# Optimization experiments

Measured on AMD Instinct MI355X. Metric: run time of the kernel, lower is better.

Reference implementation:

```python
import jax, jax.numpy as jnp
import numpy as np

N = 10000      # nodes
E = 160000     # edges (avg degree 16)
H = 128        # hidden_size
L = 3          # n_layers
NRBF = 20
RADIUS = 5.0
EPS = 1e-8
MAXZ = 100


def _xav(k, shape):
    fan_in = shape[-2]
    return jax.random.normal(k, shape, jnp.float32) / jnp.sqrt(jnp.float32(fan_in))


def setup_inputs() -> dict:
    key = jax.random.key(0)
    ks = jax.random.split(key, 12)
    return {
        "z": jax.random.randint(ks[0], (N,), 0, MAXZ, dtype=jnp.int32),
        "edge_vec": jax.random.normal(ks[1], (E, 3), jnp.float32),
        "senders": jax.random.randint(ks[2], (E,), 0, N, dtype=jnp.int32),
        "receivers": jax.random.randint(ks[3], (E,), 0, N, dtype=jnp.int32),
        "emb": jax.random.uniform(ks[4], (MAXZ, H), jnp.float32, -0.1, 0.1),
        "filt_W": _xav(ks[5], (NRBF, L * 3 * H)),
        "filt_b": jnp.zeros((L * 3 * H,), jnp.float32),
        "iW1": _xav(ks[6], (L, H, H)),
        "ib1": jnp.zeros((L, H), jnp.float32),
        "iW2": _xav(ks[7], (L, H, 3 * H)),
        "ib2": jnp.zeros((L, 3 * H), jnp.float32),
        "mW1": _xav(ks[8], (L, 2 * H, H)),
        "mb1": jnp.zeros((L, H), jnp.float32),
        "mW2": _xav(ks[9], (L, H, 3 * H)),
        "mb2": jnp.zeros((L, 3 * H), jnp.float32),
        "vW": _xav(ks[10], (L, H, 2 * H)),
    }


def _painn(z, edge_vec, senders, receivers, emb, filt_W, filt_b,
           iW1, ib1, iW2, ib2, mW1, mb1, mW2, mb2, vW):
    n = z.shape[0]
    clip = lambda x: jnp.clip(x, -1e4, 1e4)

    # edge geometry: norm + direction
    d = jnp.sqrt(jnp.sum(edge_vec ** 2, axis=-1, keepdims=True) + EPS)  # [E,1]
    dir_ij = edge_vec / d                                               # [E,3]

    # gaussian radial basis + cosine cutoff
    mu = jnp.linspace(0.0, RADIUS, NRBF)
    gamma = 0.5 / (RADIUS / NRBF) ** 2
    phi = jnp.exp(-gamma * (d - mu) ** 2)                               # [E,NRBF]
    cut = 0.5 * (jnp.cos(jnp.pi * d / RADIUS) + 1.0) * (d < RADIUS)     # [E,1]

    filters = (phi @ filt_W + filt_b) * cut                             # [E, L*3H]
    filt = jnp.split(filters, L, axis=-1)

    # embed
    s = emb[z]                                                          # [N,H]
    v = jnp.zeros((n, 3, H), dtype=s.dtype)                             # [N,3,H]

    for l in range(L):
        # ---- message ----
        x = jax.nn.silu(s @ iW1[l] + ib1[l]) @ iW2[l] + ib2[l]          # [N,3H]
        m = filt[l] * x[receivers]                                      # [E,3H]
        ds, dv1, dv2 = jnp.split(m, 3, axis=-1)
        dv = dv1[:, None, :] * dir_ij[:, :, None] + dv2[:, None, :] * v[receivers]  # [E,3,H]
        ds = jax.ops.segment_sum(ds, senders, num_segments=n)
        dv = jax.ops.segment_sum(dv, senders, num_segments=n)
        s = s + clip(ds)
        v = v + clip(dv)
        # ---- update / mixing ----
        v_l, v_r = jnp.split(v @ vW[l], 2, axis=-1)                     # [N,3,H] each
        v_norm = jnp.sqrt(jnp.sum(v_l ** 2, axis=-2) + EPS)             # [N,H]
        ts = jnp.concatenate([s, v_norm], axis=-1)                      # [N,2H]
        mm = jax.nn.silu(ts @ mW1[l] + mb1[l]) @ mW2[l] + mb2[l]        # [N,3H]
        ds2, dvu, dsv = jnp.split(mm, 3, axis=-1)
        s = s + clip(ds2 + dsv * jnp.sum(v_l * v_r, axis=1))
        v = v + clip(dvu[:, None, :] * v_r)
    return s, v


def reference(z, edge_vec, senders, receivers, emb, filt_W, filt_b,
              iW1, ib1, iW2, ib2, mW1, mb1, mW2, mb2, vW):
    return _painn(z, edge_vec, senders, receivers, emb, filt_W, filt_b,
                  iW1, ib1, iW2, ib2, mW1, mb1, mW2, mb2, vW)
```

## Files before the change

kernel.cpp:

```cpp
#include <hip/hip_runtime.h>
#include <math.h>

#define NN 10000
#define EE 160000
#define H 128
#define LAYERS 3
#define NRBF 20
#define RADIUS 5.0f
#define PI_F 3.14159265358979323846f

using f16    = _Float16;
using h2     = __attribute__((ext_vector_type(2)))  _Float16;
using half8  = __attribute__((ext_vector_type(8)))  _Float16;
using f32x16 = __attribute__((ext_vector_type(16))) float;
using u32x4  = __attribute__((ext_vector_type(4)))  unsigned int;

__device__ __forceinline__ float clipf(float x){ return fminf(fmaxf(x, -1e4f), 1e4f); }
__device__ __forceinline__ float siluf(float x){ return x / (1.0f + __expf(-x)); }

__global__ __launch_bounds__(256) void hist_kernel(const int* __restrict__ send, int* __restrict__ cnt){
    int e = blockIdx.x * 256 + threadIdx.x;
    if (e < EE) atomicAdd(&cnt[send[e]], 1);
}

__global__ __launch_bounds__(1024) void scan_kernel(const int* __restrict__ cnt,
                                                    int* __restrict__ row_ptr,
                                                    int* __restrict__ cursor){
    __shared__ int part[1024];
    int t = threadIdx.x;
    int base = t * 10;
    int local[10];
    int sum = 0;
    #pragma unroll
    for (int i = 0; i < 10; i++){
        int idx = base + i;
        local[i] = (idx < NN) ? cnt[idx] : 0;
        sum += local[i];
    }
    part[t] = sum;
    __syncthreads();
    for (int off = 1; off < 1024; off <<= 1){
        int val = (t >= off) ? part[t - off] : 0;
        __syncthreads();
        part[t] += val;
        __syncthreads();
    }
    int run = (t > 0) ? part[t-1] : 0;
    #pragma unroll
    for (int i = 0; i < 10; i++){
        int idx = base + i;
        if (idx < NN){ row_ptr[idx] = run; cursor[idx] = run; run += local[i]; }
    }
    if (t == 1023) row_ptr[NN] = part[1023];
}

__global__ __launch_bounds__(256) void build_kernel(const float* __restrict__ ev,
                                                    const int* __restrict__ send,
                                                    const int* __restrict__ recv,
                                                    int* __restrict__ cursor,
                                                    int* __restrict__ recv_s,
                                                    f16* __restrict__ Ps){
    int e = blockIdx.x * 256 + threadIdx.x;
    if (e >= EE) return;
    int p = atomicAdd(&cursor[send[e]], 1);
    recv_s[p] = recv[e];
    float x = ev[e*3+0], y = ev[e*3+1], z = ev[e*3+2];
    float d = sqrtf(x*x + y*y + z*z + 1e-8f);
    float inv = 1.0f / d;
    float cut = (d < RADIUS) ? 0.5f * (__cosf(PI_F * d / RADIUS) + 1.0f) : 0.0f;
    union { u32x4 q[3]; f16 h[24]; } o;
    #pragma unroll
    for (int k = 0; k < NRBF; k++){
        float mu = RADIUS * (float)k / (float)(NRBF - 1);
        float t = d - mu;
        o.h[k] = (f16)(__expf(-8.0f * t * t) * cut);
    }
    o.h[20] = (f16)cut;
    o.h[21] = (f16)(x*inv); o.h[22] = (f16)(y*inv); o.h[23] = (f16)(z*inv);
    u32x4* dst = (u32x4*)(Ps + (size_t)p*24);
    dst[0] = o.q[0]; dst[1] = o.q[1]; dst[2] = o.q[2];
}

__global__ __launch_bounds__(256) void wconv_kernel(const float* __restrict__ iW1, const float* __restrict__ iW2,
                                                    const float* __restrict__ vW,  const float* __restrict__ mW1,
                                                    const float* __restrict__ mW2,
                                                    f16* __restrict__ iW1T, f16* __restrict__ iW2T,
                                                    f16* __restrict__ vWT,  f16* __restrict__ mW1T,
                                                    f16* __restrict__ mW2T){
    int idx = blockIdx.x*256 + threadIdx.x;
    if (idx >= 3*180224) return;
    int l = idx / 180224;
    int r = idx % 180224;
    float val; f16* dst;
    if (r < 16384){
        int n = r >> 7, k = r & 127;
        val = iW1[l*16384 + k*128 + n]; dst = iW1T + l*16384 + r;
    } else if (r < 65536){
        int r2 = r - 16384; int n = r2 >> 7, k = r2 & 127;
        val = iW2[l*49152 + k*384 + n]; dst = iW2T + l*49152 + r2;
    } else if (r < 98304){
        int r2 = r - 65536; int n = r2 >> 7, k = r2 & 127;
        val = vW[l*32768 + k*256 + n]; dst = vWT + l*32768 + r2;
    } else if (r < 131072){
        int r2 = r - 98304; int n = r2 >> 8, k = r2 & 255;
        val = mW1[l*32768 + k*128 + n]; dst = mW1T + l*32768 + r2;
    } else {
        int r2 = r - 131072; int n = r2 >> 7, k = r2 & 127;
        val = mW2[l*49152 + k*384 + n]; dst = mW2T + l*49152 + r2;
    }
    *dst = (f16)val;
}

__global__ __launch_bounds__(256) void embed_kernel(const int* __restrict__ z,
                                                    const float* __restrict__ emb,
                                                    float* __restrict__ s, f16* __restrict__ sh){
    int idx = blockIdx.x * 256 + threadIdx.x;
    if (idx >= NN * H) return;
    int n = idx >> 7, h = idx & 127;
    float val = emb[z[n]*H + h];
    s[idx] = val;
    sh[idx] = (f16)val;
}

__global__ __launch_bounds__(256) void mlp1_kernel(const f16* __restrict__ A,
                                                   const f16* __restrict__ W1T,
                                                   const float* __restrict__ b1,
                                                   const f16* __restrict__ W2T,
                                                   const float* __restrict__ b2,
                                                   f16* __restrict__ out){
    __shared__ f16 As[64][136];
    __shared__ f16 Hs[64][136];
    int t = threadIdx.x;
    int n0 = blockIdx.x * 64;
    {
        int row = t >> 2;
        int seg0 = (t & 3) * 32;
        bool valid = (n0 + row) < NN;
        #pragma unroll
        for (int j = 0; j < 4; j++){
            int k = seg0 + j*8;
            half8 val = {};
            if (valid) val = *(const half8*)(A + (size_t)(n0+row)*128 + k);
            *(half8*)&As[row][k] = val;
        }
    }
    __syncthreads();
    int lane = t & 63, w = t >> 6;
    int koff = (lane >> 5) * 8;
    int ar = lane & 31;
    {
        int bcol = w*32 + ar;
        const f16* bp = W1T + (size_t)bcol*128 + koff;
        f32x16 acc0 = {}, acc1 = {};
        #pragma unroll
        for (int kc = 0; kc < 8; kc++){
            half8 bf = *(const half8*)(bp + kc*16);
            half8 a0 = *(const half8*)(&As[ar][koff + kc*16]);
            half8 a1 = *(const half8*)(&As[32+ar][koff + kc*16]);
            acc0 = __builtin_amdgcn_mfma_f32_32x32x16_f16(a0, bf, acc0, 0, 0, 0);
            acc1 = __builtin_amdgcn_mfma_f32_32x32x16_f16(a1, bf, acc1, 0, 0, 0);
        }
        float bv = b1[bcol];
        #pragma unroll
        for (int r = 0; r < 16; r++){
            int row = (r&3) + 8*(r>>2) + 4*(lane>>5);
            Hs[row][bcol]    = (f16)siluf(acc0[r] + bv);
            Hs[32+row][bcol] = (f16)siluf(acc1[r] + bv);
        }
    }
    __syncthreads();
    #pragma unroll
    for (int cc = 0; cc < 3; cc++){
        int bcol = (w + cc*4)*32 + ar;
        const f16* bp = W2T + (size_t)bcol*128 + koff;
        f32x16 acc0 = {}, acc1 = {};
        #pragma unroll
        for (int kc = 0; kc < 8; kc++){
            half8 bf = *(const half8*)(bp + kc*16);
            half8 a0 = *(const half8*)(&Hs[ar][koff + kc*16]);
            half8 a1 = *(const half8*)(&Hs[32+ar][koff + kc*16]);
            acc0 = __builtin_amdgcn_mfma_f32_32x32x16_f16(a0, bf, acc0, 0, 0, 0);
            acc1 = __builtin_amdgcn_mfma_f32_32x32x16_f16(a1, bf, acc1, 0, 0, 0);
        }
        float bv = b2[bcol];
        #pragma unroll
        for (int r = 0; r < 16; r++){
            int row = (r&3) + 8*(r>>2) + 4*(lane>>5);
            int g0 = n0 + row, g1 = n0 + 32 + row;
            if (g0 < NN) out[(size_t)g0*384 + bcol] = (f16)(acc0[r] + bv);
            if (g1 < NN) out[(size_t)g1*384 + bcol] = (f16)(acc1[r] + bv);
        }
    }
}

__global__ __launch_bounds__(128) void msg_kernel(const f16* __restrict__ Ps,
                                                  const int* __restrict__ recv_s,
                                                  const int* __restrict__ row_ptr,
                                                  const f16* __restrict__ xh,
                                                  const f16* __restrict__ vh,
                                                  const float* __restrict__ fW, const float* __restrict__ fb,
                                                  float* __restrict__ s, f16* __restrict__ sh,
                                                  float* __restrict__ v, f16* __restrict__ v2h, int l){
    int t = threadIdx.x;
    int lane = t & 63;
    int n = blockIdx.x * 2 + (t >> 6);
    int h0 = lane * 2;
    int col0 = l*384 + h0;
    h2 wf0[NRBF], wf1[NRBF], wf2[NRBF];
    #pragma unroll
    for (int k = 0; k < NRBF; k++){
        const float* w = fW + k*1152 + col0;
        wf0[k] = h2{(f16)w[0],   (f16)w[1]};
        wf1[k] = h2{(f16)w[128], (f16)w[129]};
        wf2[k] = h2{(f16)w[256], (f16)w[257]};
    }
    float b0x = fb[col0],     b0y = fb[col0+1];
    float b1x = fb[col0+128], b1y = fb[col0+129];
    float b2x = fb[col0+256], b2y = fb[col0+257];
    int beg = row_ptr[n], end = row_ptr[n+1];
    float ds0=0.f, ds1=0.f, dv00=0.f, dv01=0.f, dv10=0.f, dv11=0.f, dv20=0.f, dv21=0.f;
    #pragma unroll 2
    for (int idx = beg; idx < end; idx++){
        const u32x4* pp = (const u32x4*)(Ps + (size_t)idx*24);
        union { u32x4 q[3]; f16 ph[24]; } u;
        u.q[0] = pp[0]; u.q[1] = pp[1]; u.q[2] = pp[2];
        int r = recv_s[idx];
        h2 f0 = {}, f1 = {}, f2 = {};
        #pragma unroll
        for (int k = 0; k < NRBF; k++){
            f16 pk = u.ph[k];
            h2 pk2 = h2{pk, pk};
            f0 += pk2 * wf0[k];
            f1 += pk2 * wf1[k];
            f2 += pk2 * wf2[k];
        }
        float cut = (float)u.ph[20];
        float F00 = fmaf(b0x, cut, (float)f0.x), F01 = fmaf(b0y, cut, (float)f0.y);
        float F10 = fmaf(b1x, cut, (float)f1.x), F11 = fmaf(b1y, cut, (float)f1.y);
        float F20 = fmaf(b2x, cut, (float)f2.x), F21 = fmaf(b2y, cut, (float)f2.y);
        const f16* xr = xh + (size_t)r*384 + h0;
        h2 X0 = *(const h2*)xr;
        h2 X1 = *(const h2*)(xr + 128);
        h2 X2 = *(const h2*)(xr + 256);
        const f16* vp = vh + (size_t)r*128 + h0;
        h2 V0 = *(const h2*)vp;
        h2 V1 = *(const h2*)(vp + (size_t)NN*128);
        h2 V2 = *(const h2*)(vp + (size_t)2*NN*128);
        float d0 = (float)u.ph[21], d1 = (float)u.ph[22], d2 = (float)u.ph[23];
        ds0 = fmaf(F00, (float)X0.x, ds0);
        float a0 = F10 * (float)X1.x, bb0 = F20 * (float)X2.x;
        dv00 = fmaf(a0, d0, fmaf(bb0, (float)V0.x, dv00));
        dv10 = fmaf(a0, d1, fmaf(bb0, (float)V1.x, dv10));
        dv20 = fmaf(a0, d2, fmaf(bb0, (float)V2.x, dv20));
        ds1 = fmaf(F01, (float)X0.y, ds1);
        float a1 = F11 * (float)X1.y, bb1 = F21 * (float)X2.y;
        dv01 = fmaf(a1, d0, fmaf(bb1, (float)V0.y, dv01));
        dv11 = fmaf(a1, d1, fmaf(bb1, (float)V1.y, dv11));
        dv21 = fmaf(a1, d2, fmaf(bb1, (float)V2.y, dv21));
    }
    int si = n*H + h0;
    float sv0 = s[si]   + clipf(ds0);
    float sv1 = s[si+1] + clipf(ds1);
    s[si] = sv0; s[si+1] = sv1;
    *(h2*)&sh[si] = h2{(f16)sv0, (f16)sv1};
    size_t vb = (size_t)n*384 + h0;
    float nv00 = v[vb]     + clipf(dv00), nv01 = v[vb+1]   + clipf(dv01);
    float nv10 = v[vb+128] + clipf(dv10), nv11 = v[vb+129] + clipf(dv11);
    float nv20 = v[vb+256] + clipf(dv20), nv21 = v[vb+257] + clipf(dv21);
    v[vb] = nv00;     v[vb+1] = nv01;
    v[vb+128] = nv10; v[vb+129] = nv11;
    v[vb+256] = nv20; v[vb+257] = nv21;
    size_t pb = (size_t)n*128 + h0;
    *(h2*)&v2h[pb]                    = h2{(f16)nv00, (f16)nv01};
    *(h2*)&v2h[pb + (size_t)NN*128]   = h2{(f16)nv10, (f16)nv11};
    *(h2*)&v2h[pb + (size_t)2*NN*128] = h2{(f16)nv20, (f16)nv21};
}

__global__ __launch_bounds__(256) void vlr_kernel(const f16* __restrict__ v2h,
                                                  const f16* __restrict__ vWT,
                                                  f16* __restrict__ vrh,
                                                  f16* __restrict__ vnormh,
                                                  float* __restrict__ dotl){
    __shared__ f16 As[3][32][136];
    int t = threadIdx.x;
    int n0 = blockIdx.x * 32;
    for (int i = t; i < 1536; i += 256){
        int c = i / 512; int rem = i - c*512; int row = rem >> 4; int k8 = (rem & 15) * 8;
        bool valid = (n0 + row) < NN;
        half8 val = {};
        if (valid) val = *(const half8*)(v2h + ((size_t)c*NN + n0 + row)*128 + k8);
        *(half8*)&As[c][row][k8] = val;
    }
    __syncthreads();
    int lane = t & 63, w = t >> 6;
    int ar = lane & 31;
    int koff = (lane >> 5) * 8;
    int jl = w*32 + ar;
    half8 Bl[8], Br[8];
    #pragma unroll
    for (int kc = 0; kc < 8; kc++){
        Bl[kc] = *(const half8*)(vWT + (size_t)jl*128 + koff + kc*16);
        Br[kc] = *(const half8*)(vWT + (size_t)(128+jl)*128 + koff + kc*16);
    }
    f32x16 al[3], arr[3];
    #pragma unroll
    for (int c = 0; c < 3; c++){
        f32x16 accl = {}, accr = {};
        #pragma unroll
        for (int kc = 0; kc < 8; kc++){
            half8 a = *(const half8*)(&As[c][ar][koff + kc*16]);
            accl = __builtin_amdgcn_mfma_f32_32x32x16_f16(a, Bl[kc], accl, 0, 0, 0);
            accr = __builtin_amdgcn_mfma_f32_32x32x16_f16(a, Br[kc], accr, 0, 0, 0);
        }
        al[c] = accl; arr[c] = accr;
    }
    #pragma unroll
    for (int r = 0; r < 16; r++){
        int node = n0 + (r&3) + 8*(r>>2) + 4*(lane>>5);
        if (node < NN){
            float l0=al[0][r], l1=al[1][r], l2=al[2][r];
            float r0=arr[0][r], r1=arr[1][r], r2=arr[2][r];
            size_t si = (size_t)node*128 + jl;
            vnormh[si] = (f16)sqrtf(l0*l0 + l1*l1 + l2*l2 + 1e-8f);
            dotl[si]   = l0*r0 + l1*r1 + l2*r2;
            vrh[si]                    = (f16)r0;
            vrh[si + (size_t)NN*128]   = (f16)r1;
            vrh[si + (size_t)2*NN*128] = (f16)r2;
        }
    }
}

__global__ __launch_bounds__(256) void mlp2u4_kernel(const f16* __restrict__ shin,
                                                     const f16* __restrict__ vnormh,
                                                     const f16* __restrict__ W1T,
                                                     const float* __restrict__ b1,
                                                     const f16* __restrict__ W2T,
                                                     const float* __restrict__ b2,
                                                     const float* __restrict__ dotl,
                                                     const f16* __restrict__ vrh,
                                                     float* __restrict__ s, f16* __restrict__ sh,
                                                     float* __restrict__ v, f16* __restrict__ vh){
    __shared__ f16 As[64][264];
    __shared__ f16 Hs[64][136];
    int t = threadIdx.x;
    int n0 = blockIdx.x * 64;
    {
        int row = t >> 2;
        int seg0 = (t & 3) * 64;
        bool valid = (n0 + row) < NN;
        #pragma unroll
        for (int j = 0; j < 8; j++){
            int k = seg0 + j*8;
            half8 val = {};
            if (valid){
                const f16* base = (k < 128) ? shin : vnormh;
                val = *(const half8*)(base + (size_t)(n0+row)*128 + (k & 127));
            }
            *(half8*)&As[row][k] = val;
        }
    }
    __syncthreads();
    int lane = t & 63, w = t >> 6;
    int koff = (lane >> 5) * 8;
    int ar = lane & 31;
    {
        int bcol = w*32 + ar;
        const f16* bp = W1T + (size_t)bcol*256 + koff;
        f32x16 acc0 = {}, acc1 = {};
        #pragma unroll
        for (int kc = 0; kc < 16; kc++){
            half8 bf = *(const half8*)(bp + kc*16);
            half8 a0 = *(const half8*)(&As[ar][koff + kc*16]);
            half8 a1 = *(const half8*)(&As[32+ar][koff + kc*16]);
            acc0 = __builtin_amdgcn_mfma_f32_32x32x16_f16(a0, bf, acc0, 0, 0, 0);
            acc1 = __builtin_amdgcn_mfma_f32_32x32x16_f16(a1, bf, acc1, 0, 0, 0);
        }
        float bv = b1[bcol];
        #pragma unroll
        for (int r = 0; r < 16; r++){
            int row = (r&3) + 8*(r>>2) + 4*(lane>>5);
            Hs[row][bcol]    = (f16)siluf(acc0[r] + bv);
            Hs[32+row][bcol] = (f16)siluf(acc1[r] + bv);
        }
    }
    __syncthreads();
    f32x16 acc[3][2];
    #pragma unroll
    for (int cc = 0; cc < 3; cc++){
        int bcol = (w + cc*4)*32 + ar;
        const f16* bp = W2T + (size_t)bcol*128 + koff;
        f32x16 a0 = {}, a1 = {};
        #pragma unroll
        for (int kc = 0; kc < 8; kc++){
            half8 bf = *(const half8*)(bp + kc*16);
            half8 h0v = *(const half8*)(&Hs[ar][koff + kc*16]);
            half8 h1v = *(const half8*)(&Hs[32+ar][koff + kc*16]);
            a0 = __builtin_amdgcn_mfma_f32_32x32x16_f16(h0v, bf, a0, 0, 0, 0);
            a1 = __builtin_amdgcn_mfma_f32_32x32x16_f16(h1v, bf, a1, 0, 0, 0);
        }
        acc[cc][0] = a0; acc[cc][1] = a1;
    }
    int jj = w*32 + ar;
    float bv0 = b2[jj], bv1 = b2[128 + jj], bv2 = b2[256 + jj];
    #pragma unroll
    for (int rg = 0; rg < 2; rg++){
        #pragma unroll
        for (int r = 0; r < 16; r++){
            int node = n0 + rg*32 + (r&3) + 8*(r>>2) + 4*(lane>>5);
            if (node < NN){
                float m0 = acc[0][rg][r] + bv0;
                float m1 = acc[1][rg][r] + bv1;
                float m2 = acc[2][rg][r] + bv2;
                size_t si = (size_t)node*128 + jj;
                float sv = s[si] + clipf(m0 + m2*dotl[si]);
                s[si] = sv; sh[si] = (f16)sv;
                #pragma unroll
                for (int c = 0; c < 3; c++){
                    size_t pi = si + (size_t)c*NN*128;
                    float vrv = (float)vrh[pi];
                    size_t vi = (size_t)node*384 + c*128 + jj;
                    float nv = v[vi] + clipf(m1 * vrv);
                    v[vi] = nv; vh[pi] = (f16)nv;
                }
            }
        }
    }
}

extern "C" void kernel_launch(void* const* d_in, const int* in_sizes, int n_in,
                              void* d_out, int out_size, void* d_ws, size_t ws_size,
                              hipStream_t stream) {
    const int*   z    = (const int*)  d_in[0];
    const float* ev   = (const float*)d_in[1];
    const int*   send = (const int*)  d_in[2];
    const int*   recv = (const int*)  d_in[3];
    const float* emb  = (const float*)d_in[4];
    const float* fW   = (const float*)d_in[5];
    const float* fb   = (const float*)d_in[6];
    const float* iW1  = (const float*)d_in[7];
    const float* ib1  = (const float*)d_in[8];
    const float* iW2  = (const float*)d_in[9];
    const float* ib2  = (const float*)d_in[10];
    const float* mW1  = (const float*)d_in[11];
    const float* mb1  = (const float*)d_in[12];
    const float* mW2  = (const float*)d_in[13];
    const float* mb2  = (const float*)d_in[14];
    const float* vW   = (const float*)d_in[15];

    float* s = (float*)d_out;
    float* v = s + NN*H;

    char* base = (char*)d_ws;
    f16*   Ps     = (f16*)base;   base += (size_t)EE*24*2;
    int*   recvs  = (int*)base;   base += (size_t)EE*4;
    f16*   xh     = (f16*)base;   base += (size_t)NN*384*2;
    f16*   v2h    = (f16*)base;   base += (size_t)3*NN*128*2;
    f16*   vh     = (f16*)base;   base += (size_t)3*NN*128*2;
    f16*   vrh    = (f16*)base;   base += (size_t)3*NN*128*2;
    f16*   vnormh = (f16*)base;   base += (size_t)NN*128*2;
    float* dotl   = (float*)base; base += (size_t)NN*128*4;
    f16*   sh     = (f16*)base;   base += (size_t)NN*128*2;
    f16*   iW1T   = (f16*)base;   base += (size_t)3*16384*2;
    f16*   iW2T   = (f16*)base;   base += (size_t)3*49152*2;
    f16*   vWT    = (f16*)base;   base += (size_t)3*32768*2;
    f16*   mW1T   = (f16*)base;   base += (size_t)3*32768*2;
    f16*   mW2T   = (f16*)base;   base += (size_t)3*49152*2;
    int* cnt      = (int*)base;   base += (size_t)NN*4;
    int* row_ptr  = (int*)base;   base += (size_t)(NN+1)*4;
    int* cursor   = (int*)base;

    hipMemsetAsync(cnt, 0, NN*sizeof(int), stream);
    hist_kernel<<<(EE+255)/256, 256, 0, stream>>>(send, cnt);
    scan_kernel<<<1, 1024, 0, stream>>>(cnt, row_ptr, cursor);
    build_kernel<<<(EE+255)/256, 256, 0, stream>>>(ev, send, recv, cursor, recvs, Ps);
    wconv_kernel<<<(3*180224+255)/256, 256, 0, stream>>>(iW1, iW2, vW, mW1, mW2,
                                                         iW1T, iW2T, vWT, mW1T, mW2T);
    embed_kernel<<<(NN*H+255)/256, 256, 0, stream>>>(z, emb, s, sh);
    hipMemsetAsync(v,  0, (size_t)NN*384*sizeof(float), stream);
    hipMemsetAsync(vh, 0, (size_t)3*NN*128*sizeof(f16), stream);

    const int MB  = (NN + 63) / 64;
    const int VB  = (NN + 31) / 32;

    for (int l = 0; l < LAYERS; l++){
        mlp1_kernel<<<MB, 256, 0, stream>>>(sh, iW1T + l*16384, ib1 + l*H,
                                            iW2T + l*49152, ib2 + l*384, xh);
        msg_kernel<<<NN/2, 128, 0, stream>>>(Ps, recvs, row_ptr, xh, vh, fW, fb, s, sh, v, v2h, l);
        vlr_kernel<<<VB, 256, 0, stream>>>(v2h, vWT + l*32768, vrh, vnormh, dotl);
        mlp2u4_kernel<<<MB, 256, 0, stream>>>(sh, vnormh, mW1T + l*32768, mb1 + l*H,
                                              mW2T + l*49152, mb2 + l*384,
                                              dotl, vrh, s, sh, v, vh);
    }
}
```

Before: 412.3 us.

## Fuse vector projection and update MLP into one kernel; shrink MLP node tile

Merges vlr_kernel and mlp2u4_kernel into a single vmix_kernel. The v@vW results (v_norm, v_l·v_r dot, v_r) stay in registers and shared memory instead of going through global buffers. This removes one launch per layer and the write and re-read of vrh, vnormh and dotl. mlp1 and the fused kernel now use 32-node tiles instead of 64, which doubles the block count but halves per-block reuse of weights loaded from global memory. The fused kernel also holds many more live registers, which may lower occupancy.

```diff
diff --git a/kernel.cpp b/kernel.cpp
--- a/kernel.cpp
+++ b/kernel.cpp
@@ -128,44 +128,35 @@
                                                    const f16* __restrict__ W2T,
                                                    const float* __restrict__ b2,
                                                    f16* __restrict__ out){
-    __shared__ f16 As[64][136];
-    __shared__ f16 Hs[64][136];
+    __shared__ f16 As[32][136];
+    __shared__ f16 Hs[32][136];
     int t = threadIdx.x;
-    int n0 = blockIdx.x * 64;
-    {
-        int row = t >> 2;
-        int seg0 = (t & 3) * 32;
-        bool valid = (n0 + row) < NN;
-        #pragma unroll
-        for (int j = 0; j < 4; j++){
-            int k = seg0 + j*8;
-            half8 val = {};
-            if (valid) val = *(const half8*)(A + (size_t)(n0+row)*128 + k);
-            *(half8*)&As[row][k] = val;
-        }
+    int n0 = blockIdx.x * 32;
+    for (int i = t; i < 512; i += 256){
+        int row = i >> 4, k8 = (i & 15) * 8;
+        half8 val = {};
+        if (n0 + row < NN) val = *(const half8*)(A + (size_t)(n0+row)*128 + k8);
+        *(half8*)&As[row][k8] = val;
     }
     __syncthreads();
     int lane = t & 63, w = t >> 6;
+    int ar = lane & 31;
     int koff = (lane >> 5) * 8;
-    int ar = lane & 31;
     {
         int bcol = w*32 + ar;
         const f16* bp = W1T + (size_t)bcol*128 + koff;
-        f32x16 acc0 = {}, acc1 = {};
+        f32x16 acc = {};
         #pragma unroll
         for (int kc = 0; kc < 8; kc++){
             half8 bf = *(const half8*)(bp + kc*16);
-            half8 a0 = *(const half8*)(&As[ar][koff + kc*16]);
-            half8 a1 = *(const half8*)(&As[32+ar][koff + kc*16]);
-            acc0 = __builtin_amdgcn_mfma_f32_32x32x16_f16(a0, bf, acc0, 0, 0, 0);
-            acc1 = __builtin_amdgcn_mfma_f32_32x32x16_f16(a1, bf, acc1, 0, 0, 0);
+            half8 a  = *(const half8*)(&As[ar][koff + kc*16]);
+            acc = __builtin_amdgcn_mfma_f32_32x32x16_f16(a, bf, acc, 0, 0, 0);
         }
         float bv = b1[bcol];
         #pragma unroll
         for (int r = 0; r < 16; r++){
             int row = (r&3) + 8*(r>>2) + 4*(lane>>5);
-            Hs[row][bcol]    = (f16)siluf(acc0[r] + bv);
-            Hs[32+row][bcol] = (f16)siluf(acc1[r] + bv);
+            Hs[row][bcol] = (f16)siluf(acc[r] + bv);
         }
     }
     __syncthreads();
@@ -173,22 +164,19 @@
     for (int cc = 0; cc < 3; cc++){
         int bcol = (w + cc*4)*32 + ar;
         const f16* bp = W2T + (size_t)bcol*128 + koff;
-        f32x16 acc0 = {}, acc1 = {};
+        f32x16 acc = {};
         #pragma unroll
         for (int kc = 0; kc < 8; kc++){
             half8 bf = *(const half8*)(bp + kc*16);
-            half8 a0 = *(const half8*)(&Hs[ar][koff + kc*16]);
-            half8 a1 = *(const half8*)(&Hs[32+ar][koff + kc*16]);
-            acc0 = __builtin_amdgcn_mfma_f32_32x32x16_f16(a0, bf, acc0, 0, 0, 0);
-            acc1 = __builtin_amdgcn_mfma_f32_32x32x16_f16(a1, bf, acc1, 0, 0, 0);
+            half8 a  = *(const half8*)(&Hs[ar][koff + kc*16]);
+            acc = __builtin_amdgcn_mfma_f32_32x32x16_f16(a, bf, acc, 0, 0, 0);
         }
         float bv = b2[bcol];
         #pragma unroll
         for (int r = 0; r < 16; r++){
             int row = (r&3) + 8*(r>>2) + 4*(lane>>5);
-            int g0 = n0 + row, g1 = n0 + 32 + row;
-            if (g0 < NN) out[(size_t)g0*384 + bcol] = (f16)(acc0[r] + bv);
-            if (g1 < NN) out[(size_t)g1*384 + bcol] = (f16)(acc1[r] + bv);
+            int g = n0 + row;
+            if (g < NN) out[(size_t)g*384 + bcol] = (f16)(acc[r] + bv);
         }
     }
 }
@@ -276,153 +264,116 @@
     *(h2*)&v2h[pb + (size_t)2*NN*128] = h2{(f16)nv20, (f16)nv21};
 }
 
-__global__ __launch_bounds__(256) void vlr_kernel(const f16* __restrict__ v2h,
-                                                  const f16* __restrict__ vWT,
-                                                  f16* __restrict__ vrh,
-                                                  f16* __restrict__ vnormh,
-                                                  float* __restrict__ dotl){
-    __shared__ f16 As[3][32][136];
+__global__ __launch_bounds__(256) void vmix_kernel(const f16* __restrict__ v2h,
+                                                   const f16* __restrict__ sh_in,
+                                                   const f16* __restrict__ vWT,
+                                                   const f16* __restrict__ W1T,
+                                                   const float* __restrict__ b1,
+                                                   const f16* __restrict__ W2T,
+                                                   const float* __restrict__ b2,
+                                                   float* __restrict__ s, f16* __restrict__ sh,
+                                                   float* __restrict__ v, f16* __restrict__ vh){
+    __shared__ f16 As3[3][32][136];
+    __shared__ f16 ts[32][264];
+    __shared__ f16 Hs[32][136];
     int t = threadIdx.x;
     int n0 = blockIdx.x * 32;
     for (int i = t; i < 1536; i += 256){
         int c = i / 512; int rem = i - c*512; int row = rem >> 4; int k8 = (rem & 15) * 8;
-        bool valid = (n0 + row) < NN;
         half8 val = {};
-        if (valid) val = *(const half8*)(v2h + ((size_t)c*NN + n0 + row)*128 + k8);
-        *(half8*)&As[c][row][k8] = val;
+        if (n0 + row < NN) val = *(const half8*)(v2h + ((size_t)c*NN + n0 + row)*128 + k8);
+        *(half8*)&As3[c][row][k8] = val;
+    }
+    for (int i = t; i < 512; i += 256){
+        int row = i >> 4, k8 = (i & 15) * 8;
+        half8 val = {};
+        if (n0 + row < NN) val = *(const half8*)(sh_in + (size_t)(n0+row)*128 + k8);
+        *(half8*)&ts[row][k8] = val;
     }
     __syncthreads();
     int lane = t & 63, w = t >> 6;
     int ar = lane & 31;
     int koff = (lane >> 5) * 8;
     int jl = w*32 + ar;
-    half8 Bl[8], Br[8];
-    #pragma unroll
-    for (int kc = 0; kc < 8; kc++){
-        Bl[kc] = *(const half8*)(vWT + (size_t)jl*128 + koff + kc*16);
-        Br[kc] = *(const half8*)(vWT + (size_t)(128+jl)*128 + koff + kc*16);
-    }
     f32x16 al[3], arr[3];
     #pragma unroll
     for (int c = 0; c < 3; c++){
         f32x16 accl = {}, accr = {};
         #pragma unroll
         for (int kc = 0; kc < 8; kc++){
-            half8 a = *(const half8*)(&As[c][ar][koff + kc*16]);
-            accl = __builtin_amdgcn_mfma_f32_32x32x16_f16(a, Bl[kc], accl, 0, 0, 0);
-            accr = __builtin_amdgcn_mfma_f32_32x32x16_f16(a, Br[kc], accr, 0, 0, 0);
+            half8 bl = *(const half8*)(vWT + (size_t)jl*128 + koff + kc*16);
+            half8 br = *(const half8*)(vWT + (size_t)(128+jl)*128 + koff + kc*16);
+            half8 a  = *(const half8*)(&As3[c][ar][koff + kc*16]);
+            accl = __builtin_amdgcn_mfma_f32_32x32x16_f16(a, bl, accl, 0, 0, 0);
+            accr = __builtin_amdgcn_mfma_f32_32x32x16_f16(a, br, accr, 0, 0, 0);
         }
         al[c] = accl; arr[c] = accr;
     }
+    float dot[16], vr0[16], vr1[16], vr2[16];
+    #pragma unroll
+    for (int r = 0; r < 16; r++){
+        int row = (r&3) + 8*(r>>2) + 4*(lane>>5);
+        float l0=al[0][r], l1=al[1][r], l2=al[2][r];
+        float r0=arr[0][r], r1=arr[1][r], r2=arr[2][r];
+        ts[row][128 + jl] = (f16)sqrtf(l0*l0 + l1*l1 + l2*l2 + 1e-8f);
+        dot[r] = l0*r0 + l1*r1 + l2*r2;
+        vr0[r] = r0; vr1[r] = r1; vr2[r] = r2;
+    }
+    __syncthreads();
+    {
+        int bcol = w*32 + ar;
+        const f16* bp = W1T + (size_t)bcol*256 + koff;
+        f32x16 acc = {};
+        #pragma unroll
+        for (int kc = 0; kc < 16; kc++){
+            half8 bf = *(const half8*)(bp + kc*16);
+            half8 a  = *(const half8*)(&ts[ar][koff + kc*16]);
+            acc = __builtin_amdgcn_mfma_f32_32x32x16_f16(a, bf, acc, 0, 0, 0);
+        }
+        float bv = b1[bcol];
+        #pragma unroll
+        for (int r = 0; r < 16; r++){
+            int row = (r&3) + 8*(r>>2) + 4*(lane>>5);
+            Hs[row][bcol] = (f16)siluf(acc[r] + bv);
+        }
+    }
+    __syncthreads();
+    f32x16 macc[3];
+    #pragma unroll
+    for (int cc = 0; cc < 3; cc++){
+        int bcol = (w + cc*4)*32 + ar;
+        const f16* bp = W2T + (size_t)bcol*128 + koff;
+        f32x16 acc = {};
+        #pragma unroll
+        for (int kc = 0; kc < 8; kc++){
+            half8 bf = *(const half8*)(bp + kc*16);
+            half8 a  = *(const half8*)(&Hs[ar][koff + kc*16]);
+            acc = __builtin_amdgcn_mfma_f32_32x32x16_f16(a, bf, acc, 0, 0, 0);
+        }
+        macc[cc] = acc;
+    }
+    int jj = w*32 + ar;
+    float bv0 = b2[jj], bv1 = b2[128 + jj], bv2 = b2[256 + jj];
     #pragma unroll
     for (int r = 0; r < 16; r++){
         int node = n0 + (r&3) + 8*(r>>2) + 4*(lane>>5);
         if (node < NN){
-            float l0=al[0][r], l1=al[1][r], l2=al[2][r];
-            float r0=arr[0][r], r1=arr[1][r], r2=arr[2][r];
-            size_t si = (size_t)node*128 + jl;
-            vnormh[si] = (f16)sqrtf(l0*l0 + l1*l1 + l2*l2 + 1e-8f);
-            dotl[si]   = l0*r0 + l1*r1 + l2*r2;
-            vrh[si]                    = (f16)r0;
-            vrh[si + (size_t)NN*128]   = (f16)r1;
-            vrh[si + (size_t)2*NN*128] = (f16)r2;
-        }
-    }
-}
-
-__global__ __launch_bounds__(256) void mlp2u4_kernel(const f16* __restrict__ shin,
-                                                     const f16* __restrict__ vnormh,
-                                                     const f16* __restrict__ W1T,
-                                                     const float* __restrict__ b1,
-                                                     const f16* __restrict__ W2T,
-                                                     const float* __restrict__ b2,
-                                                     const float* __restrict__ dotl,
-                                                     const f16* __restrict__ vrh,
-                                                     float* __restrict__ s, f16* __restrict__ sh,
-                                                     float* __restrict__ v, f16* __restrict__ vh){
-    __shared__ f16 As[64][264];
-    __shared__ f16 Hs[64][136];
-    int t = threadIdx.x;
-    int n0 = blockIdx.x * 64;
-    {
-        int row = t >> 2;
-        int seg0 = (t & 3) * 64;
-        bool valid = (n0 + row) < NN;
-        #pragma unroll
-        for (int j = 0; j < 8; j++){
-            int k = seg0 + j*8;
-            half8 val = {};
-            if (valid){
-                const f16* base = (k < 128) ? shin : vnormh;
-                val = *(const half8*)(base + (size_t)(n0+row)*128 + (k & 127));
-            }
-            *(half8*)&As[row][k] = val;
-        }
-    }
-    __syncthreads();
-    int lane = t & 63, w = t >> 6;
-    int koff = (lane >> 5) * 8;
-    int ar = lane & 31;
-    {
-        int bcol = w*32 + ar;
-        const f16* bp = W1T + (size_t)bcol*256 + koff;
-        f32x16 acc0 = {}, acc1 = {};
-        #pragma unroll
-        for (int kc = 0; kc < 16; kc++){
-            half8 bf = *(const half8*)(bp + kc*16);
-            half8 a0 = *(const half8*)(&As[ar][koff + kc*16]);
-            half8 a1 = *(const half8*)(&As[32+ar][koff + kc*16]);
-            acc0 = __builtin_amdgcn_mfma_f32_32x32x16_f16(a0, bf, acc0, 0, 0, 0);
-            acc1 = __builtin_amdgcn_mfma_f32_32x32x16_f16(a1, bf, acc1, 0, 0, 0);
-        }
-        float bv = b1[bcol];
-        #pragma unroll
-        for (int r = 0; r < 16; r++){
-            int row = (r&3) + 8*(r>>2) + 4*(lane>>5);
-            Hs[row][bcol]    = (f16)siluf(acc0[r] + bv);
-            Hs[32+row][bcol] = (f16)siluf(acc1[r] + bv);
-        }
-    }
-    __syncthreads();
-    f32x16 acc[3][2];
-    #pragma unroll
-    for (int cc = 0; cc < 3; cc++){
-        int bcol = (w + cc*4)*32 + ar;
-        const f16* bp = W2T + (size_t)bcol*128 + koff;
-        f32x16 a0 = {}, a1 = {};
-        #pragma unroll
-        for (int kc = 0; kc < 8; kc++){
-            half8 bf = *(const half8*)(bp + kc*16);
-            half8 h0v = *(const half8*)(&Hs[ar][koff + kc*16]);
-            half8 h1v = *(const half8*)(&Hs[32+ar][koff + kc*16]);
-            a0 = __builtin_amdgcn_mfma_f32_32x32x16_f16(h0v, bf, a0, 0, 0, 0);
-            a1 = __builtin_amdgcn_mfma_f32_32x32x16_f16(h1v, bf, a1, 0, 0, 0);
-        }
-        acc[cc][0] = a0; acc[cc][1] = a1;
-    }
-    int jj = w*32 + ar;
-    float bv0 = b2[jj], bv1 = b2[128 + jj], bv2 = b2[256 + jj];
-    #pragma unroll
-    for (int rg = 0; rg < 2; rg++){
-        #pragma unroll
-        for (int r = 0; r < 16; r++){
-            int node = n0 + rg*32 + (r&3) + 8*(r>>2) + 4*(lane>>5);
-            if (node < NN){
-                float m0 = acc[0][rg][r] + bv0;
-                float m1 = acc[1][rg][r] + bv1;
-                float m2 = acc[2][rg][r] + bv2;
-                size_t si = (size_t)node*128 + jj;
-                float sv = s[si] + clipf(m0 + m2*dotl[si]);
-                s[si] = sv; sh[si] = (f16)sv;
-                #pragma unroll
-                for (int c = 0; c < 3; c++){
-                    size_t pi = si + (size_t)c*NN*128;
-                    float vrv = (float)vrh[pi];
-                    size_t vi = (size_t)node*384 + c*128 + jj;
-                    float nv = v[vi] + clipf(m1 * vrv);
-                    v[vi] = nv; vh[pi] = (f16)nv;
-                }
-            }
+            float m0 = macc[0][r] + bv0;
+            float m1 = macc[1][r] + bv1;
+            float m2 = macc[2][r] + bv2;
+            size_t si = (size_t)node*128 + jj;
+            float sv = s[si] + clipf(m0 + m2*dot[r]);
+            s[si] = sv; sh[si] = (f16)sv;
+            size_t vi = (size_t)node*384 + jj;
+            float nv0 = v[vi]       + clipf(m1 * vr0[r]);
+            float nv1 = v[vi + 128] + clipf(m1 * vr1[r]);
+            float nv2 = v[vi + 256] + clipf(m1 * vr2[r]);
+            v[vi]       = nv0;
+            v[vi + 128] = nv1;
+            v[vi + 256] = nv2;
+            vh[si]                    = (f16)nv0;
+            vh[si + (size_t)NN*128]   = (f16)nv1;
+            vh[si + (size_t)2*NN*128] = (f16)nv2;
         }
     }
 }
@@ -456,9 +407,6 @@
     f16*   xh     = (f16*)base;   base += (size_t)NN*384*2;
     f16*   v2h    = (f16*)base;   base += (size_t)3*NN*128*2;
     f16*   vh     = (f16*)base;   base += (size_t)3*NN*128*2;
-    f16*   vrh    = (f16*)base;   base += (size_t)3*NN*128*2;
-    f16*   vnormh = (f16*)base;   base += (size_t)NN*128*2;
-    float* dotl   = (float*)base; base += (size_t)NN*128*4;
     f16*   sh     = (f16*)base;   base += (size_t)NN*128*2;
     f16*   iW1T   = (f16*)base;   base += (size_t)3*16384*2;
     f16*   iW2T   = (f16*)base;   base += (size_t)3*49152*2;
@@ -479,16 +427,15 @@
     hipMemsetAsync(v,  0, (size_t)NN*384*sizeof(float), stream);
     hipMemsetAsync(vh, 0, (size_t)3*NN*128*sizeof(f16), stream);
 
-    const int MB  = (NN + 63) / 64;
-    const int VB  = (NN + 31) / 32;
+    const int MB32 = (NN + 31) / 32;
 
     for (int l = 0; l < LAYERS; l++){
-        mlp1_kernel<<<MB, 256, 0, stream>>>(sh, iW1T + l*16384, ib1 + l*H,
-                                            iW2T + l*49152, ib2 + l*384, xh);
+        mlp1_kernel<<<MB32, 256, 0, stream>>>(sh, iW1T + l*16384, ib1 + l*H,
+                                              iW2T + l*49152, ib2 + l*384, xh);
         msg_kernel<<<NN/2, 128, 0, stream>>>(Ps, recvs, row_ptr, xh, vh, fW, fb, s, sh, v, v2h, l);
-        vlr_kernel<<<VB, 256, 0, stream>>>(v2h, vWT + l*32768, vrh, vnormh, dotl);
-        mlp2u4_kernel<<<MB, 256, 0, stream>>>(sh, vnormh, mW1T + l*32768, mb1 + l*H,
+        vmix_kernel<<<MB32, 256, 0, stream>>>(v2h, sh, vWT + l*32768,
+                                              mW1T + l*32768, mb1 + l*H,
                                               mW2T + l*49152, mb2 + l*384,
-                                              dotl, vrh, s, sh, v, vh);
-    }
-}
+                                              s, sh, v, vh);
+    }
+}
```

After: 373.8 us, median of 2. -9.3%, faster.
